# Optimization experiments

Hardware: AMD Instinct MI355X
Metric: run time of the kernel (lower is better)

The kernel has to match this reference:

```python
import jax, jax.numpy as jnp
import numpy as np

N_NODES = 200000
N_GRAPHS = 4000


def _sage_conv(x, src, dst, W_l, b_l, W_r, num_nodes):
    # PyG SAGEConv (aggr='mean'): out = lin_l(mean_{j in N(i)} x_j) + lin_r(x_i)
    msg_sum = jax.ops.segment_sum(x[src], dst, num_segments=num_nodes)      # [N, d]
    deg = jax.ops.segment_sum(jnp.ones_like(src, dtype=x.dtype), dst,
                              num_segments=num_nodes)                       # [N]
    mean_nbr = msg_sum / jnp.maximum(deg, 1.0)[:, None]
    return mean_nbr @ W_l.T + b_l + x @ W_r.T


def setup_inputs() -> dict:
    key = jax.random.key(0)
    ks = jax.random.split(key, 10)
    in_ch, hid, out = 32, 64, 2
    E = 3200000
    x = jax.random.normal(ks[0], (N_NODES, in_ch), dtype=jnp.float32)
    edge_index = jax.random.randint(ks[1], (2, E), 0, N_NODES, dtype=jnp.int64)
    batch = jnp.sort(jax.random.randint(ks[2], (N_NODES,), 0, N_GRAPHS, dtype=jnp.int64))

    def glorot(k, shape):
        lim = 1.0 / np.sqrt(shape[1])
        return jax.random.uniform(k, shape, jnp.float32, -lim, lim)

    return {
        "x": x,
        "edge_index": edge_index,
        "batch": batch,
        "W1_l": glorot(ks[3], (hid, in_ch)),
        "b1": jnp.zeros((hid,), jnp.float32),
        "W1_r": glorot(ks[4], (hid, in_ch)),
        "W2_l": glorot(ks[5], (hid, hid)),
        "b2": jnp.zeros((hid,), jnp.float32),
        "W2_r": glorot(ks[6], (hid, hid)),
        "W_lin": glorot(ks[7], (out, hid)),
        "b_lin": jnp.zeros((out,), jnp.float32),
    }


def reference(x, edge_index, batch, W1_l, b1, W1_r, W2_l, b2, W2_r, W_lin, b_lin):
    src, dst = edge_index[0], edge_index[1]
    h = jax.nn.relu(_sage_conv(x, src, dst, W1_l, b1, W1_r, N_NODES))
    h = jax.nn.relu(_sage_conv(h, src, dst, W2_l, b2, W2_r, N_NODES))
    # global_mean_pool over graph ids
    pool_sum = jax.ops.segment_sum(h, batch, num_segments=N_GRAPHS)          # [G, 64]
    cnt = jax.ops.segment_sum(jnp.ones_like(batch, dtype=h.dtype), batch,
                              num_segments=N_GRAPHS)                          # [G]
    pooled = pool_sum / jnp.maximum(cnt, 1.0)[:, None]
    return pooled @ W_lin.T + b_lin
```

## Files before the change

kernel.cpp:

```cpp
#include <hip/hip_runtime.h>
#include <hip/hip_bf16.h>


#define WS_ALIGN 64
#define EPB 4096
#define BSHIFT 10
#define BNODES 1024
#define BCAP 20480

typedef short bf16x8 __attribute__((ext_vector_type(8)));
typedef float f32x4 __attribute__((ext_vector_type(4)));

__device__ inline unsigned short f2bf(float f) {
    unsigned u = __float_as_uint(f);
    return (unsigned short)((u + 0x7fffu + ((u >> 16) & 1u)) >> 16);
}

__device__ inline void acc8(const uint4 u, float* a) {
    a[0] += __uint_as_float(u.x << 16);
    a[1] += __uint_as_float(u.x & 0xffff0000u);
    a[2] += __uint_as_float(u.y << 16);
    a[3] += __uint_as_float(u.y & 0xffff0000u);
    a[4] += __uint_as_float(u.z << 16);
    a[5] += __uint_as_float(u.z & 0xffff0000u);
    a[6] += __uint_as_float(u.w << 16);
    a[7] += __uint_as_float(u.w & 0xffff0000u);
}


__global__ void prep_kernel(const float* __restrict__ x, unsigned short* __restrict__ xb,
                            const int* __restrict__ batch, int* __restrict__ cnt,
                            const float* __restrict__ W1_l, const float* __restrict__ W1_r,
                            const float* __restrict__ W2_l, const float* __restrict__ W2_r,
                            unsigned short* __restrict__ whi1, unsigned short* __restrict__ whi2,
                            int* __restrict__ bucketCursor,
                            int N, int NB, int total4) {
    const int gid = blockIdx.x * blockDim.x + threadIdx.x;
    if (gid < total4) {
        const float4 v = reinterpret_cast<const float4*>(x)[gid];
        ushort4 o;
        o.x = f2bf(v.x); o.y = f2bf(v.y); o.z = f2bf(v.z); o.w = f2bf(v.w);
        reinterpret_cast<ushort4*>(xb)[gid] = o;
    }
    if (gid < N) atomicAdd(&cnt[batch[gid]], 1);
    if (gid < NB) bucketCursor[gid] = gid * BCAP;
    if (gid < 64 * 64) {
        const int o = gid >> 6, k = gid & 63;
        const float v = (k < 32) ? W1_l[o * 32 + k] : W1_r[o * 32 + (k - 32)];
        whi1[gid] = f2bf(v);
    }
    if (gid < 64 * 128) {
        const int o = gid >> 7, k = gid & 127;
        const float v = (k < 64) ? W2_l[o * 64 + k] : W2_r[o * 64 + (k - 64)];
        whi2[gid] = f2bf(v);
    }
}


__global__ __launch_bounds__(256) void bucket_scatter_kernel(const int* __restrict__ src,
                                                             const int* __restrict__ dst,
                                                             int* __restrict__ bucketCursor,
                                                             unsigned* __restrict__ bucketData,
                                                             int E, int NB) {
    __shared__ int hist[256];
    __shared__ int cur[256];
    const int t = threadIdx.x;
    hist[t] = 0;
    __syncthreads();
    const int eBase = blockIdx.x * EPB + t;
    int s[16], b[16], dl[16];
#pragma unroll
    for (int j = 0; j < 16; ++j) {
        int e = eBase + j * 256;
        if (e < E) {
            int d = dst[e];
            s[j]  = src[e];
            b[j]  = d >> BSHIFT;
            dl[j] = d & (BNODES - 1);
            atomicAdd(&hist[b[j]], 1);
        } else {
            b[j] = -1;
        }
    }
    __syncthreads();
    if (t < NB && hist[t] > 0) cur[t] = atomicAdd(&bucketCursor[t], hist[t]);
    __syncthreads();
#pragma unroll
    for (int j = 0; j < 16; ++j) {
        if (b[j] >= 0) {
            int pos = atomicAdd(&cur[b[j]], 1);
            if (pos < (b[j] + 1) * BCAP)
                bucketData[pos] = ((unsigned)s[j] << BSHIFT) | (unsigned)dl[j];
        }
    }
}

__global__ __launch_bounds__(256) void csr_build_kernel(const unsigned* __restrict__ bucketData,
                                                        const int* __restrict__ bucketCursor,
                                                        int* __restrict__ offs,
                                                        int* __restrict__ offe,
                                                        int* __restrict__ csr_src,
                                                        int N) {
    __shared__ int cnt[BNODES];
    __shared__ int sscan[256];
    __shared__ int cur[BNODES];
    const int t   = threadIdx.x;
    const int bkt = blockIdx.x;
    const int nodeBase = bkt << BSHIFT;
    const int regionBase = bkt * BCAP;
    const int count = min(bucketCursor[bkt] - regionBase, BCAP);
    for (int i = t; i < BNODES; i += 256) cnt[i] = 0;
    __syncthreads();
    for (int k = regionBase + t; k < regionBase + count; k += 256)
        atomicAdd(&cnt[bucketData[k] & (BNODES - 1)], 1);
    __syncthreads();
    int local[4];
    int sum = 0;
#pragma unroll
    for (int j = 0; j < 4; ++j) { local[j] = sum; sum += cnt[t * 4 + j]; }
    sscan[t] = sum;
    __syncthreads();
    for (int off = 1; off < 256; off <<= 1) {
        int v = (t >= off) ? sscan[t - off] : 0;
        __syncthreads();
        sscan[t] += v;
        __syncthreads();
    }
    int base = (t > 0) ? sscan[t - 1] : 0;
#pragma unroll
    for (int j = 0; j < 4; ++j) cur[t * 4 + j] = base + local[j];
    __syncthreads();
    for (int i = t; i < BNODES; i += 256) {
        const int node = nodeBase + i;
        if (node < N) {
            offs[node] = regionBase + cur[i];
            offe[node] = regionBase + cur[i] + cnt[i];
        }
    }
    __syncthreads();
    for (int k = regionBase + t; k < regionBase + count; k += 256) {
        const unsigned v = bucketData[k];
        const int d = (int)(v & (BNODES - 1));
        const int pos = regionBase + atomicAdd(&cur[d], 1);
        csr_src[pos] = (int)(v >> BSHIFT);
    }
}


template <int D>
__global__ void agg_bf16_kernel(const unsigned short* __restrict__ featb,
                                const int* __restrict__ csr_src,
                                const int* __restrict__ offs,
                                const int* __restrict__ offe,
                                unsigned short* __restrict__ aggb, int N) {
    constexpr int TPN = D / 8;
    int tid  = blockIdx.x * blockDim.x + threadIdx.x;
    int node = tid / TPN;
    int part = tid % TPN;
    if (node >= N) return;
    const int beg = offs[node];
    const int end = offe[node];
    const uint4* base = reinterpret_cast<const uint4*>(featb);
    float a[8] = {0.f, 0.f, 0.f, 0.f, 0.f, 0.f, 0.f, 0.f};
    int k = beg;
    for (; k + 8 <= end; k += 8) {
        int s[8];
#pragma unroll
        for (int j = 0; j < 8; ++j) s[j] = csr_src[k + j];
        uint4 u[8];
#pragma unroll
        for (int j = 0; j < 8; ++j) u[j] = base[(size_t)s[j] * TPN + part];
#pragma unroll
        for (int j = 0; j < 8; ++j) acc8(u[j], a);
    }
    for (; k + 4 <= end; k += 4) {
        const int s0 = csr_src[k + 0];
        const int s1 = csr_src[k + 1];
        const int s2 = csr_src[k + 2];
        const int s3 = csr_src[k + 3];
        const uint4 u0 = base[(size_t)s0 * TPN + part];
        const uint4 u1 = base[(size_t)s1 * TPN + part];
        const uint4 u2 = base[(size_t)s2 * TPN + part];
        const uint4 u3 = base[(size_t)s3 * TPN + part];
        acc8(u0, a); acc8(u1, a); acc8(u2, a); acc8(u3, a);
    }
    for (; k < end; ++k) {
        const uint4 u = base[(size_t)csr_src[k] * TPN + part];
        acc8(u, a);
    }
    const float inv = 1.0f / fmaxf((float)(end - beg), 1.0f);
    ushort4 lo, hi;
    lo.x = f2bf(a[0] * inv); lo.y = f2bf(a[1] * inv);
    lo.z = f2bf(a[2] * inv); lo.w = f2bf(a[3] * inv);
    hi.x = f2bf(a[4] * inv); hi.y = f2bf(a[5] * inv);
    hi.z = f2bf(a[6] * inv); hi.w = f2bf(a[7] * inv);
    unsigned short* dstp = aggb + (size_t)node * D + part * 8;
    *reinterpret_cast<ushort4*>(dstp)     = lo;
    *reinterpret_cast<ushort4*>(dstp + 4) = hi;
}


template <int DIN, bool POOL>
__launch_bounds__(256)
__global__ void mfma_dense_kernel(const unsigned short* __restrict__ aggb,
                                  const unsigned short* __restrict__ xinb,
                                  const unsigned short* __restrict__ whi,
                                  const float* __restrict__ bias,
                                  unsigned short* __restrict__ houtb,
                                  const int* __restrict__ batch,
                                  float* __restrict__ pool_sum,
                                  int N, int nSteps) {
    constexpr int K   = 2 * DIN;
    constexpr int STR = K + 8;
    constexpr int D8  = DIN / 8;
    constexpr int K8  = K / 8;
    __shared__ unsigned short A_s[64 * STR];
    __shared__ unsigned short Bh_s[64 * STR];
    const int tid = threadIdx.x;
    const int nodeBase = blockIdx.x * 64;

    for (int i = tid; i < 64 * D8 * 2; i += 256) {
        const int half = i / (64 * D8);
        const int j = i % (64 * D8);
        const int node = j / D8, q = j % D8;
        const int n = min(nodeBase + node, N - 1);
        const unsigned short* srcp = half ? xinb : aggb;
        const uint4 u = *reinterpret_cast<const uint4*>(srcp + (size_t)n * DIN + q * 8);
        *reinterpret_cast<uint4*>(&A_s[node * STR + half * DIN + q * 8]) = u;
    }
    for (int i = tid; i < 64 * K8; i += 256) {
        const int o = i / K8, q = i % K8;
        const uint4 u = *reinterpret_cast<const uint4*>(whi + (size_t)o * K + q * 8);
        *reinterpret_cast<uint4*>(&Bh_s[o * STR + q * 8]) = u;
    }
    __syncthreads();

    const int lane = tid & 63;
    const int wave = tid >> 6;
    const int lr = lane & 15;
    const int q  = lane >> 4;
    f32x4 acc[4];
#pragma unroll
    for (int t = 0; t < 4; ++t) {
        const float b = bias[t * 16 + lr];
        acc[t] = (f32x4){b, b, b, b};
    }
    const unsigned short* Arow = &A_s[(wave * 16 + lr) * STR + q * 8];
    for (int s = 0; s < nSteps; ++s) {
        const bf16x8 af = *reinterpret_cast<const bf16x8*>(Arow + s * 32);
#pragma unroll
        for (int t = 0; t < 4; ++t) {
            const bf16x8 bh = *reinterpret_cast<const bf16x8*>(
                &Bh_s[(t * 16 + lr) * STR + s * 32 + q * 8]);
            acc[t] = __builtin_amdgcn_mfma_f32_16x16x32_bf16(af, bh, acc[t], 0, 0, 0);
        }
    }

    if (POOL) {
        float ag[4] = {0.f, 0.f, 0.f, 0.f};
        int gcur = -1;
        for (int reg = 0; reg < 4; ++reg) {
            const int n = nodeBase + wave * 16 + q * 4 + reg;
            if (n >= N) break;
            const int g = batch[n];
            if (g != gcur) {
                if (gcur >= 0) {
#pragma unroll
                    for (int t = 0; t < 4; ++t)
                        atomicAdd(&pool_sum[(size_t)gcur * 64 + t * 16 + lr], ag[t]);
                }
                gcur = g;
                ag[0] = ag[1] = ag[2] = ag[3] = 0.f;
            }
#pragma unroll
            for (int t = 0; t < 4; ++t)
                ag[t] += fmaxf(acc[t][reg], 0.0f);
        }
        if (gcur >= 0) {
#pragma unroll
            for (int t = 0; t < 4; ++t)
                atomicAdd(&pool_sum[(size_t)gcur * 64 + t * 16 + lr], ag[t]);
        }
    } else {
        for (int reg = 0; reg < 4; ++reg) {
            const int n = nodeBase + wave * 16 + q * 4 + reg;
            if (n >= N) break;
#pragma unroll
            for (int t = 0; t < 4; ++t)
                houtb[(size_t)n * 64 + t * 16 + lr] = f2bf(fmaxf(acc[t][reg], 0.0f));
        }
    }
}


__global__ void final_kernel(const float* __restrict__ pool_sum,
                             const int* __restrict__ cnt,
                             const float* __restrict__ W_lin,
                             const float* __restrict__ b_lin,
                             float* __restrict__ out, int G) {
    int t = blockIdx.x * blockDim.x + threadIdx.x;
    if (t >= G * 2) return;
    int g = t >> 1, o = t & 1;
    float inv = 1.0f / fmaxf((float)cnt[g], 1.0f);
    float acc = b_lin[o];
#pragma unroll
    for (int c = 0; c < 64; ++c)
        acc = fmaf(pool_sum[(size_t)g * 64 + c] * inv, W_lin[o * 64 + c], acc);
    out[t] = acc;
}

extern "C" void kernel_launch(void* const* d_in, const int* in_sizes, int n_in,
                              void* d_out, int out_size, void* d_ws, size_t ws_size,
                              hipStream_t stream) {
    const float* x     = (const float*)d_in[0];
    const int*   ei    = (const int*)d_in[1];
    const int*   batch = (const int*)d_in[2];
    const float* W1_l  = (const float*)d_in[3];
    const float* b1    = (const float*)d_in[4];
    const float* W1_r  = (const float*)d_in[5];
    const float* W2_l  = (const float*)d_in[6];
    const float* b2    = (const float*)d_in[7];
    const float* W2_r  = (const float*)d_in[8];
    const float* W_lin = (const float*)d_in[9];
    const float* b_lin = (const float*)d_in[10];

    const int N = in_sizes[0] / 32;
    const int E = in_sizes[1] / 2;
    const int G = out_size / 2;
    const int* src = ei;
    const int* dst = ei + E;
    const int NB = (N + BNODES - 1) >> BSHIFT;

    char* p = (char*)d_ws;
    auto carve = [&](size_t bytes) -> void* {
        void* r = (void*)p;
        p += (bytes + (WS_ALIGN - 1)) / WS_ALIGN * WS_ALIGN;
        return r;
    };
    int*            bucketCursor = (int*)carve(256 * 4);
    unsigned*       bucketData   = (unsigned*)carve((size_t)NB * BCAP * 4);
    int*            offs         = (int*)carve((size_t)N * 4);
    int*            offe         = (int*)carve((size_t)N * 4);
    int*            csr_src      = (int*)carve((size_t)NB * BCAP * 4);
    unsigned short* xb           = (unsigned short*)carve((size_t)N * 32 * 2);
    unsigned short* aggb         = (unsigned short*)carve((size_t)N * 64 * 2);
    unsigned short* h1b          = (unsigned short*)carve((size_t)N * 64 * 2);
    unsigned short* whi1         = (unsigned short*)carve(64 * 64 * 2);
    unsigned short* whi2         = (unsigned short*)carve(64 * 128 * 2);
    float*          pool         = (float*)carve((size_t)G * 64 * 4);
    int*            cnt          = (int*)carve((size_t)G * 4);
    float*          out          = (float*)d_out;

    hipMemsetAsync(pool, 0, (size_t)G * 64 * 4, stream);
    hipMemsetAsync(cnt, 0, (size_t)G * 4, stream);

    const int TB = 256;
    const int total4 = N * 32 / 4;
    prep_kernel<<<(total4 + TB - 1) / TB, TB, 0, stream>>>(
        x, xb, batch, cnt, W1_l, W1_r, W2_l, W2_r, whi1, whi2,
        bucketCursor, N, NB, total4);
    bucket_scatter_kernel<<<(E + EPB - 1) / EPB, TB, 0, stream>>>(src, dst, bucketCursor,
                                                                  bucketData, E, NB);
    csr_build_kernel<<<NB, TB, 0, stream>>>(bucketData, bucketCursor, offs, offe, csr_src, N);

    agg_bf16_kernel<32><<<((size_t)N * 4 + TB - 1) / TB, TB, 0, stream>>>(
        xb, csr_src, offs, offe, aggb, N);
    mfma_dense_kernel<32, false><<<(N + 63) / 64, TB, 0, stream>>>(
        aggb, xb, whi1, b1, h1b, nullptr, nullptr, N, 2);

    agg_bf16_kernel<64><<<((size_t)N * 8 + TB - 1) / TB, TB, 0, stream>>>(
        h1b, csr_src, offs, offe, aggb, N);
    mfma_dense_kernel<64, true><<<(N + 63) / 64, TB, 0, stream>>>(
        aggb, h1b, whi2, b2, nullptr, batch, pool, N, 4);

    final_kernel<<<(G * 2 + TB - 1) / TB, TB, 0, stream>>>(pool, cnt, W_lin, b_lin, out, G);
}
```

Measured before the change: 377.6 us.

## Shrink CSR buckets, drop memsets and derive graph counts by binary search

```diff
diff --git a/kernel.cpp b/kernel.cpp
--- a/kernel.cpp
+++ b/kernel.cpp
@@ -4,9 +4,10 @@
 
 #define WS_ALIGN 64
 #define EPB 4096
-#define BSHIFT 10
-#define BNODES 1024
-#define BCAP 20480
+#define BSHIFT 8
+#define BNODES 256
+#define BCAP 6144
+#define MAXNB 1024
 
 typedef short bf16x8 __attribute__((ext_vector_type(8)));
 typedef float f32x4 __attribute__((ext_vector_type(4)));
@@ -29,12 +30,11 @@
 
 
 __global__ void prep_kernel(const float* __restrict__ x, unsigned short* __restrict__ xb,
-                            const int* __restrict__ batch, int* __restrict__ cnt,
                             const float* __restrict__ W1_l, const float* __restrict__ W1_r,
                             const float* __restrict__ W2_l, const float* __restrict__ W2_r,
                             unsigned short* __restrict__ whi1, unsigned short* __restrict__ whi2,
-                            int* __restrict__ bucketCursor,
-                            int N, int NB, int total4) {
+                            int* __restrict__ bucketCursor, float* __restrict__ pool,
+                            int N, int NB, int G, int total4) {
     const int gid = blockIdx.x * blockDim.x + threadIdx.x;
     if (gid < total4) {
         const float4 v = reinterpret_cast<const float4*>(x)[gid];
@@ -42,8 +42,8 @@
         o.x = f2bf(v.x); o.y = f2bf(v.y); o.z = f2bf(v.z); o.w = f2bf(v.w);
         reinterpret_cast<ushort4*>(xb)[gid] = o;
     }
-    if (gid < N) atomicAdd(&cnt[batch[gid]], 1);
     if (gid < NB) bucketCursor[gid] = gid * BCAP;
+    if (gid < G * 64) pool[gid] = 0.0f;
     if (gid < 64 * 64) {
         const int o = gid >> 6, k = gid & 63;
         const float v = (k < 32) ? W1_l[o * 32 + k] : W1_r[o * 32 + (k - 32)];
@@ -62,10 +62,10 @@
                                                              int* __restrict__ bucketCursor,
                                                              unsigned* __restrict__ bucketData,
                                                              int E, int NB) {
-    __shared__ int hist[256];
-    __shared__ int cur[256];
+    __shared__ int hist[MAXNB];
+    __shared__ int cur[MAXNB];
     const int t = threadIdx.x;
-    hist[t] = 0;
+    for (int i = t; i < MAXNB; i += 256) hist[i] = 0;
     __syncthreads();
     const int eBase = blockIdx.x * EPB + t;
     int s[16], b[16], dl[16];
@@ -83,7 +83,8 @@
         }
     }
     __syncthreads();
-    if (t < NB && hist[t] > 0) cur[t] = atomicAdd(&bucketCursor[t], hist[t]);
+    for (int bb = t; bb < NB; bb += 256)
+        if (hist[bb] > 0) cur[bb] = atomicAdd(&bucketCursor[bb], hist[bb]);
     __syncthreads();
 #pragma unroll
     for (int j = 0; j < 16; ++j) {
@@ -102,23 +103,20 @@
                                                         int* __restrict__ csr_src,
                                                         int N) {
     __shared__ int cnt[BNODES];
-    __shared__ int sscan[256];
+    __shared__ int sscan[BNODES];
     __shared__ int cur[BNODES];
     const int t   = threadIdx.x;
     const int bkt = blockIdx.x;
     const int nodeBase = bkt << BSHIFT;
     const int regionBase = bkt * BCAP;
     const int count = min(bucketCursor[bkt] - regionBase, BCAP);
-    for (int i = t; i < BNODES; i += 256) cnt[i] = 0;
+    cnt[t] = 0;
     __syncthreads();
     for (int k = regionBase + t; k < regionBase + count; k += 256)
         atomicAdd(&cnt[bucketData[k] & (BNODES - 1)], 1);
     __syncthreads();
-    int local[4];
-    int sum = 0;
-#pragma unroll
-    for (int j = 0; j < 4; ++j) { local[j] = sum; sum += cnt[t * 4 + j]; }
-    sscan[t] = sum;
+    int v0 = cnt[t];
+    sscan[t] = v0;
     __syncthreads();
     for (int off = 1; off < 256; off <<= 1) {
         int v = (t >= off) ? sscan[t - off] : 0;
@@ -126,16 +124,12 @@
         sscan[t] += v;
         __syncthreads();
     }
-    int base = (t > 0) ? sscan[t - 1] : 0;
-#pragma unroll
-    for (int j = 0; j < 4; ++j) cur[t * 4 + j] = base + local[j];
-    __syncthreads();
-    for (int i = t; i < BNODES; i += 256) {
-        const int node = nodeBase + i;
-        if (node < N) {
-            offs[node] = regionBase + cur[i];
-            offe[node] = regionBase + cur[i] + cnt[i];
-        }
+    const int excl = sscan[t] - v0;
+    cur[t] = excl;
+    const int node = nodeBase + t;
+    if (node < N) {
+        offs[node] = regionBase + excl;
+        offe[node] = regionBase + excl + v0;
     }
     __syncthreads();
     for (int k = regionBase + t; k < regionBase + count; k += 256) {
@@ -293,15 +287,26 @@
 }
 
 
+__device__ inline int lower_bound_batch(const int* __restrict__ batch, int N, int key) {
+    int lo = 0, hi = N;
+    while (lo < hi) {
+        const int mid = (lo + hi) >> 1;
+        if (batch[mid] < key) lo = mid + 1; else hi = mid;
+    }
+    return lo;
+}
+
 __global__ void final_kernel(const float* __restrict__ pool_sum,
-                             const int* __restrict__ cnt,
+                             const int* __restrict__ batch,
                              const float* __restrict__ W_lin,
                              const float* __restrict__ b_lin,
-                             float* __restrict__ out, int G) {
+                             float* __restrict__ out, int G, int N) {
     int t = blockIdx.x * blockDim.x + threadIdx.x;
     if (t >= G * 2) return;
     int g = t >> 1, o = t & 1;
-    float inv = 1.0f / fmaxf((float)cnt[g], 1.0f);
+    const int c0 = lower_bound_batch(batch, N, g);
+    const int c1 = lower_bound_batch(batch, N, g + 1);
+    float inv = 1.0f / fmaxf((float)(c1 - c0), 1.0f);
     float acc = b_lin[o];
 #pragma unroll
     for (int c = 0; c < 64; ++c)
@@ -337,7 +342,7 @@
         p += (bytes + (WS_ALIGN - 1)) / WS_ALIGN * WS_ALIGN;
         return r;
     };
-    int*            bucketCursor = (int*)carve(256 * 4);
+    int*            bucketCursor = (int*)carve((size_t)MAXNB * 4);
     unsigned*       bucketData   = (unsigned*)carve((size_t)NB * BCAP * 4);
     int*            offs         = (int*)carve((size_t)N * 4);
     int*            offe         = (int*)carve((size_t)N * 4);
@@ -348,17 +353,13 @@
     unsigned short* whi1         = (unsigned short*)carve(64 * 64 * 2);
     unsigned short* whi2         = (unsigned short*)carve(64 * 128 * 2);
     float*          pool         = (float*)carve((size_t)G * 64 * 4);
-    int*            cnt          = (int*)carve((size_t)G * 4);
     float*          out          = (float*)d_out;
-
-    hipMemsetAsync(pool, 0, (size_t)G * 64 * 4, stream);
-    hipMemsetAsync(cnt, 0, (size_t)G * 4, stream);
 
     const int TB = 256;
     const int total4 = N * 32 / 4;
     prep_kernel<<<(total4 + TB - 1) / TB, TB, 0, stream>>>(
-        x, xb, batch, cnt, W1_l, W1_r, W2_l, W2_r, whi1, whi2,
-        bucketCursor, N, NB, total4);
+        x, xb, W1_l, W1_r, W2_l, W2_r, whi1, whi2, bucketCursor, pool,
+        N, NB, G, total4);
     bucket_scatter_kernel<<<(E + EPB - 1) / EPB, TB, 0, stream>>>(src, dst, bucketCursor,
                                                                   bucketData, E, NB);
     csr_build_kernel<<<NB, TB, 0, stream>>>(bucketData, bucketCursor, offs, offe, csr_src, N);
@@ -373,5 +374,6 @@
     mfma_dense_kernel<64, true><<<(N + 63) / 64, TB, 0, stream>>>(
         aggb, h1b, whi2, b2, nullptr, batch, pool, N, 4);
 
-    final_kernel<<<(G * 2 + TB - 1) / TB, TB, 0, stream>>>(pool, cnt, W_lin, b_lin, out, G);
-}
+    final_kernel<<<(G * 2 + TB - 1) / TB, TB, 0, stream>>>(pool, batch, W_lin, b_lin,
+                                                           out, G, N);
+}
```

Measured after the change: 357.7 us (median of 2 runs). 5.3% less time.
